# Performance work log

Measured on AMD Instinct MI355X. Metric: run time of the kernel, lower is better.

Reference implementation:

```python
import jax, jax.numpy as jnp
import numpy as np

B, S, D, H = 4, 1024, 512, 8
HD = D // H          # head_dim = 64
WIN = 32
EMB_HID = 128
NEG = -1e10


def _rel_coords_log():
    # __make_pair_wise_relative_positions: 2D meshgrid over window indexes
    idx = jnp.arange(WIN)
    coords = jnp.stack(jnp.meshgrid(idx, idx, indexing='ij'), 0).reshape(2, -1)  # [2, S]
    rel = coords[:, :, None] - coords[:, None, :]                                # [2, S, S]
    rel = rel.transpose(1, 2, 0).reshape(-1, 2).astype(jnp.float32)              # [S*S, 2]
    return jnp.sign(rel) * jnp.log1p(jnp.abs(rel))


def setup_inputs() -> dict:
    key = jax.random.key(0)
    ks = jax.random.split(key, 16)
    sd = 1.0 / np.sqrt(D)
    p = lambda k, sh, s: (jax.random.normal(k, sh, jnp.float32) * s)
    return {
        'query': jax.random.normal(ks[0], (B, S, D), jnp.float32),
        'key':   jax.random.normal(ks[1], (B, S, D), jnp.float32),
        'value': jax.random.normal(ks[2], (B, S, D), jnp.float32),
        'mask':  jnp.ones((B, 1, 1, S), jnp.int64),
        'Wq': p(ks[3], (D, D), sd), 'bq': jnp.zeros((D,), jnp.float32),
        'Wk': p(ks[4], (D, D), sd), 'bk': jnp.zeros((D,), jnp.float32),
        'Wv': p(ks[5], (D, D), sd), 'bv': jnp.zeros((D,), jnp.float32),
        'Wo': p(ks[6], (D, D), sd), 'bo': jnp.zeros((D,), jnp.float32),
        'W1': p(ks[7], (2, EMB_HID), 0.7), 'b1': jnp.zeros((EMB_HID,), jnp.float32),
        'W2': p(ks[8], (EMB_HID, H), 0.1), 'b2': jnp.zeros((H,), jnp.float32),
    }


def reference(query, key, value, mask, Wq, bq, Wk, bk, Wv, bv, Wo, bo, W1, b1, W2, b2):
    scale = jnp.sqrt(jnp.float32(HD))
    Q = (query @ Wq + bq).reshape(B, S, H, HD).transpose(0, 2, 1, 3)  # [B,H,S,HD]
    K = (key   @ Wk + bk).reshape(B, S, H, HD).transpose(0, 2, 1, 3)
    V = (value @ Wv + bv).reshape(B, S, H, HD).transpose(0, 2, 1, 3)

    energy = jnp.einsum('bhqd,bhkd->bhqk', Q, K) / scale             # [B,H,S,S]

    # continuous position bias: MLP(2 -> EMB_HID -> H) on log-spaced rel coords
    rel = _rel_coords_log()                                           # [S*S, 2]
    bias = jax.nn.relu(rel @ W1 + b1) @ W2 + b2                       # [S*S, H]
    bias = bias.T.reshape(H, S, S)[None]                              # [1,H,S,S]
    energy = energy + bias

    energy = jnp.where(mask == 0, NEG, energy)
    attention = jax.nn.softmax(energy, axis=-1)                       # [B,H,S,S]
    x = jnp.einsum('bhqk,bhkd->bhqd', attention, V)                   # dropout p=0
    x = x.transpose(0, 2, 1, 3).reshape(B, S, D)
    x = x @ Wo + bo
    return x, attention
```

## Files before the change

kernel.cpp:

```cpp
#include <hip/hip_runtime.h>
#include <hip/hip_bf16.h>

typedef __attribute__((ext_vector_type(4))) float f32x4;
typedef __attribute__((ext_vector_type(8))) short bf16x8;
typedef __attribute__((ext_vector_type(4))) unsigned short u16x4;

#define DEVI __device__ __forceinline__

constexpr int B_ = 4, S_ = 1024, D_ = 512, H_ = 8, HD_ = 64;
constexpr float CSH = 11.0903548f;

DEVI unsigned short f2b(float f) {
  union { float f; unsigned u; } v; v.f = f;
  unsigned r = v.u + 0x7fffu + ((v.u >> 16) & 1u);
  return (unsigned short)(r >> 16);
}

__global__ __launch_bounds__(256) void k_prep(const float* Wa, const float* Wb,
                                              const float* Wc, const float* Wd,
                                              unsigned short* T0, unsigned short* T1,
                                              unsigned short* T2, unsigned short* T3,
                                              const float* mW1, const float* mb1,
                                              const float* mW2, const float* mb2,
                                              float* table) {
  if (blockIdx.z == 4) {
    if (blockIdx.y != 0) return;
    int idx = blockIdx.x * 256 + threadIdx.x;
    if (idx >= 63 * 63) return;
    int dy = idx / 63 - 31, dx = idx % 63 - 31;
    float r0 = copysignf(log1pf(fabsf((float)dy)), (float)dy);
    float r1 = copysignf(log1pf(fabsf((float)dx)), (float)dx);
    float acc[8];
#pragma unroll
    for (int h = 0; h < 8; ++h) acc[h] = mb2[h];
    for (int j = 0; j < 128; ++j) {
      float hv = fmaxf(r0 * mW1[j] + r1 * mW1[128 + j] + mb1[j], 0.f);
#pragma unroll
      for (int h = 0; h < 8; ++h) acc[h] += hv * mW2[j * 8 + h];
    }
#pragma unroll
    for (int h = 0; h < 8; ++h) table[h * 3969 + idx] = acc[h] - CSH;
    return;
  }
  const float* W = blockIdx.z == 0 ? Wa : blockIdx.z == 1 ? Wb : blockIdx.z == 2 ? Wc : Wd;
  unsigned short* T = blockIdx.z == 0 ? T0 : blockIdx.z == 1 ? T1 : blockIdx.z == 2 ? T2 : T3;
  __shared__ float tile[32][33];
  int tx = threadIdx.x & 31, ty = threadIdx.x >> 5;
  int n0 = blockIdx.x * 32, k0 = blockIdx.y * 32;
#pragma unroll
  for (int r = 0; r < 4; ++r) tile[ty + r * 8][tx] = W[(size_t)(k0 + ty + r * 8) * D_ + n0 + tx];
  __syncthreads();
#pragma unroll
  for (int r = 0; r < 4; ++r) T[(size_t)(n0 + ty + r * 8) * D_ + k0 + tx] = f2b(tile[tx][ty + r * 8]);
}

__global__ __launch_bounds__(256) void k_gemm_qkv(const float* Aq, const float* Ak, const float* Av,
                                                  const unsigned short* Tq, const unsigned short* Tk,
                                                  const unsigned short* Tv,
                                                  const float* bqv, const float* bkv, const float* bvv,
                                                  unsigned short* Oq, unsigned short* Ok,
                                                  unsigned short* OvT) {
  const float* A = blockIdx.z == 0 ? Aq : blockIdx.z == 1 ? Ak : Av;
  const unsigned short* BT = blockIdx.z == 0 ? Tq : blockIdx.z == 1 ? Tk : Tv;
  const float* bias = blockIdx.z == 0 ? bqv : blockIdx.z == 1 ? bkv : bvv;

  __shared__ unsigned short As[64][72];
  __shared__ unsigned short Bs[128][72];
  const int tid = threadIdx.x;
  const int lane = tid & 63, wave = tid >> 6;
  const int lr = lane & 15, lg = lane >> 4;
  const int wm = (wave >> 1) * 32, wn = (wave & 1) * 64;
  const int m0 = blockIdx.x * 64, n0 = blockIdx.y * 128;

  f32x4 acc[2][4];
#pragma unroll
  for (int i = 0; i < 2; ++i)
#pragma unroll
    for (int j = 0; j < 4; ++j) acc[i][j] = (f32x4){0.f, 0.f, 0.f, 0.f};

  for (int k0 = 0; k0 < 512; k0 += 64) {
#pragma unroll
    for (int i = 0; i < 4; ++i) {
      int idx = tid + i * 256;
      int r = idx >> 4, c4 = (idx & 15) * 4;
      float4 fv = *(const float4*)(A + (size_t)(m0 + r) * 512 + k0 + c4);
      u16x4 wv;
      wv[0] = f2b(fv.x); wv[1] = f2b(fv.y); wv[2] = f2b(fv.z); wv[3] = f2b(fv.w);
      *(u16x4*)&As[r][c4] = wv;
    }
#pragma unroll
    for (int i = 0; i < 8; ++i) {
      int idx = tid + i * 256;
      int r = idx >> 4, c4 = (idx & 15) * 4;
      *(u16x4*)&Bs[r][c4] = *(const u16x4*)(BT + (size_t)(n0 + r) * 512 + k0 + c4);
    }
    __syncthreads();
#pragma unroll
    for (int kk = 0; kk < 2; ++kk) {
      bf16x8 af[2], bg[4];
#pragma unroll
      for (int i = 0; i < 2; ++i) af[i] = *(const bf16x8*)&As[wm + i * 16 + lr][kk * 32 + lg * 8];
#pragma unroll
      for (int j = 0; j < 4; ++j) bg[j] = *(const bf16x8*)&Bs[wn + j * 16 + lr][kk * 32 + lg * 8];
#pragma unroll
      for (int i = 0; i < 2; ++i)
#pragma unroll
        for (int j = 0; j < 4; ++j)
          acc[i][j] = __builtin_amdgcn_mfma_f32_16x16x32_bf16(af[i], bg[j], acc[i][j], 0, 0, 0);
    }
    __syncthreads();
  }

#pragma unroll
  for (int i = 0; i < 2; ++i)
#pragma unroll
    for (int j = 0; j < 4; ++j) {
      int mbase = m0 + wm + i * 16 + lg * 4;
      int n = n0 + wn + j * 16 + lr;
      float bvl = bias[n];
      int h = n >> 6, hd = n & 63;
      int bseg = mbase >> 10, s0 = mbase & 1023;
      if (blockIdx.z == 2) {
        u16x4 pk;
#pragma unroll
        for (int r = 0; r < 4; ++r) pk[r] = f2b(acc[i][j][r] + bvl);
        *(u16x4*)(OvT + (((size_t)(bseg * H_ + h) * 64 + hd) * 1024 + s0)) = pk;
      } else {
        unsigned short* outp = blockIdx.z == 0 ? Oq : Ok;
#pragma unroll
        for (int r = 0; r < 4; ++r) {
          float v = acc[i][j][r] + bvl;
          outp[(((size_t)bseg * H_ + h) * S_ + s0 + r) * HD_ + hd] = f2b(v);
        }
      }
    }
}

__global__ __launch_bounds__(256) void k_gemm_out(const unsigned short* A, const unsigned short* BT,
                                                  const float* bias, float* outp) {
  __shared__ unsigned short As[64][72];
  __shared__ unsigned short Bs[128][72];
  const int tid = threadIdx.x;
  const int lane = tid & 63, wave = tid >> 6;
  const int lr = lane & 15, lg = lane >> 4;
  const int wm = (wave >> 1) * 32, wn = (wave & 1) * 64;
  const int m0 = blockIdx.x * 64, n0 = blockIdx.y * 128;

  f32x4 acc[2][4];
#pragma unroll
  for (int i = 0; i < 2; ++i)
#pragma unroll
    for (int j = 0; j < 4; ++j) acc[i][j] = (f32x4){0.f, 0.f, 0.f, 0.f};

  for (int k0 = 0; k0 < 512; k0 += 64) {
#pragma unroll
    for (int i = 0; i < 4; ++i) {
      int idx = tid + i * 256;
      int r = idx >> 4, c4 = (idx & 15) * 4;
      *(u16x4*)&As[r][c4] = *(const u16x4*)(A + (size_t)(m0 + r) * 512 + k0 + c4);
    }
#pragma unroll
    for (int i = 0; i < 8; ++i) {
      int idx = tid + i * 256;
      int r = idx >> 4, c4 = (idx & 15) * 4;
      *(u16x4*)&Bs[r][c4] = *(const u16x4*)(BT + (size_t)(n0 + r) * 512 + k0 + c4);
    }
    __syncthreads();
#pragma unroll
    for (int kk = 0; kk < 2; ++kk) {
      bf16x8 af[2], bg[4];
#pragma unroll
      for (int i = 0; i < 2; ++i) af[i] = *(const bf16x8*)&As[wm + i * 16 + lr][kk * 32 + lg * 8];
#pragma unroll
      for (int j = 0; j < 4; ++j) bg[j] = *(const bf16x8*)&Bs[wn + j * 16 + lr][kk * 32 + lg * 8];
#pragma unroll
      for (int i = 0; i < 2; ++i)
#pragma unroll
        for (int j = 0; j < 4; ++j)
          acc[i][j] = __builtin_amdgcn_mfma_f32_16x16x32_bf16(af[i], bg[j], acc[i][j], 0, 0, 0);
    }
    __syncthreads();
  }

#pragma unroll
  for (int i = 0; i < 2; ++i)
#pragma unroll
    for (int j = 0; j < 4; ++j) {
      int mbase = m0 + wm + i * 16 + lg * 4;
      int n = n0 + wn + j * 16 + lr;
      float bvl = bias[n];
#pragma unroll
      for (int r = 0; r < 4; ++r)
        outp[(size_t)(mbase + r) * 512 + n] = acc[i][j][r] + bvl;
    }
}

__global__ __launch_bounds__(256) void k_attn(const unsigned short* Qb, const unsigned short* Kb,
                                              const unsigned short* VT, const float* tbl,
                                              const int* mask, float* out_attn,
                                              unsigned short* Xp) {
  const int tid = threadIdx.x;
  const int lane = tid & 63, w = tid >> 6;
  const int lr = lane & 15, lg = lane >> 4;
  const int bh = blockIdx.y, b = bh >> 3, h = bh & 7;
  const int q0 = blockIdx.x * 64;

  __shared__ unsigned short Ks[2][64][64];
  __shared__ unsigned short Vt[2][64][64];
  __shared__ unsigned short Pl[4][16][64];
  __shared__ float biasT[3969];
  __shared__ float mbig[1024];
  __shared__ int tbad[16];

  const unsigned short* Qh = Qb + (size_t)bh * (S_ * HD_);
  const unsigned short* Kh = Kb + (size_t)bh * (S_ * HD_);
  const unsigned short* Vth = VT + (size_t)bh * (HD_ * S_);

  const int srow = tid >> 3, sc = tid & 7;
  const int swz = (sc ^ (srow & 7)) * 8;

  if (tid < 16) tbad[tid] = 0;
  __syncthreads();
  for (int i = tid; i < 3969; i += 256) biasT[i] = tbl[h * 3969 + i];
  {
    int4 mv = *(const int4*)(mask + b * S_ + tid * 4);
    int base = tid * 4;
    mbig[base] = mv.x ? 3.0e38f : -1.0e9f;
    mbig[base + 1] = mv.y ? 3.0e38f : -1.0e9f;
    mbig[base + 2] = mv.z ? 3.0e38f : -1.0e9f;
    mbig[base + 3] = mv.w ? 3.0e38f : -1.0e9f;
    if (!(mv.x && mv.y && mv.z && mv.w)) tbad[base >> 6] = 1;
  }
  *(bf16x8*)&Ks[0][srow][swz] = *(const bf16x8*)(Kh + (size_t)srow * 64 + sc * 8);
  *(bf16x8*)&Ks[0][srow + 32][swz] = *(const bf16x8*)(Kh + (size_t)(srow + 32) * 64 + sc * 8);

  const int qrow = q0 + w * 16 + lr;
  const bf16x8 bq0 = *(const bf16x8*)(Qh + (size_t)qrow * 64 + lg * 8);
  const bf16x8 bq1 = *(const bf16x8*)(Qh + (size_t)qrow * 64 + 32 + lg * 8);
  const int qterm = (qrow >> 5) * 63 + (qrow & 31) + 1984;

  float ls = 0.f;
  __syncthreads();

  for (int kt = 0; kt < 16; ++kt) {
    const int cur = kt & 1;
    bf16x8 nk0, nk1;
    if (kt < 15) {
      nk0 = *(const bf16x8*)(Kh + (size_t)((kt + 1) * 64 + srow) * 64 + sc * 8);
      nk1 = *(const bf16x8*)(Kh + (size_t)((kt + 1) * 64 + srow + 32) * 64 + sc * 8);
    }
    const int bidx = qterm - 126 * kt;
    const bool bad = tbad[kt] != 0;
#pragma unroll
    for (int fn = 0; fn < 4; ++fn) {
      const unsigned short* krow = &Ks[cur][fn * 16 + lr][0];
      bf16x8 a0 = *(const bf16x8*)(krow + (lg ^ (lr & 7)) * 8);
      bf16x8 a1 = *(const bf16x8*)(krow + ((4 + lg) ^ (lr & 7)) * 8);
      f32x4 s = (f32x4){0.f, 0.f, 0.f, 0.f};
      s = __builtin_amdgcn_mfma_f32_16x16x32_bf16(a0, bq0, s, 0, 0, 0);
      s = __builtin_amdgcn_mfma_f32_16x16x32_bf16(a1, bq1, s, 0, 0, 0);
      const int kob = fn * 16 + lg * 4;
      const int ib = bidx - kob - (fn >= 2 ? 31 : 0);
#pragma unroll
      for (int r = 0; r < 4; ++r) {
        float arg = fmaf(s[r], 0.125f, biasT[ib - r]);
        if (bad) arg = fminf(arg, mbig[kt * 64 + kob + r]);
        ls += __expf(arg);
      }
    }
    if (kt < 15) {
      *(bf16x8*)&Ks[cur ^ 1][srow][swz] = nk0;
      *(bf16x8*)&Ks[cur ^ 1][srow + 32][swz] = nk1;
    }
    __syncthreads();
  }
  ls += __shfl_xor(ls, 16, 64);
  ls += __shfl_xor(ls, 32, 64);
  const float inv = 1.f / ls;

  f32x4 of[4];
#pragma unroll
  for (int i = 0; i < 4; ++i) of[i] = (f32x4){0.f, 0.f, 0.f, 0.f};
  float* oa = out_attn + (size_t)bh * (S_ * S_) + (size_t)qrow * S_;

  *(bf16x8*)&Ks[0][srow][swz] = *(const bf16x8*)(Kh + (size_t)srow * 64 + sc * 8);
  *(bf16x8*)&Ks[0][srow + 32][swz] = *(const bf16x8*)(Kh + (size_t)(srow + 32) * 64 + sc * 8);
  *(bf16x8*)&Vt[0][srow][swz] = *(const bf16x8*)(Vth + (size_t)srow * S_ + sc * 8);
  *(bf16x8*)&Vt[0][srow + 32][swz] = *(const bf16x8*)(Vth + (size_t)(srow + 32) * S_ + sc * 8);
  __syncthreads();

  for (int kt = 0; kt < 16; ++kt) {
    const int cur = kt & 1;
    bf16x8 nk0, nk1, nv0, nv1;
    if (kt < 15) {
      nk0 = *(const bf16x8*)(Kh + (size_t)((kt + 1) * 64 + srow) * 64 + sc * 8);
      nk1 = *(const bf16x8*)(Kh + (size_t)((kt + 1) * 64 + srow + 32) * 64 + sc * 8);
      nv0 = *(const bf16x8*)(Vth + (size_t)srow * S_ + (kt + 1) * 64 + sc * 8);
      nv1 = *(const bf16x8*)(Vth + (size_t)(srow + 32) * S_ + (kt + 1) * 64 + sc * 8);
    }
    const int bidx = qterm - 126 * kt;
    const bool bad = tbad[kt] != 0;
#pragma unroll
    for (int fn = 0; fn < 4; ++fn) {
      const unsigned short* krow = &Ks[cur][fn * 16 + lr][0];
      bf16x8 a0 = *(const bf16x8*)(krow + (lg ^ (lr & 7)) * 8);
      bf16x8 a1 = *(const bf16x8*)(krow + ((4 + lg) ^ (lr & 7)) * 8);
      f32x4 s = (f32x4){0.f, 0.f, 0.f, 0.f};
      s = __builtin_amdgcn_mfma_f32_16x16x32_bf16(a0, bq0, s, 0, 0, 0);
      s = __builtin_amdgcn_mfma_f32_16x16x32_bf16(a1, bq1, s, 0, 0, 0);
      const int kob = fn * 16 + lg * 4;
      const int ib = bidx - kob - (fn >= 2 ? 31 : 0);
      f32x4 pr;
      u16x4 pb;
#pragma unroll
      for (int r = 0; r < 4; ++r) {
        float arg = fmaf(s[r], 0.125f, biasT[ib - r]);
        if (bad) arg = fminf(arg, mbig[kt * 64 + kob + r]);
        float p = __expf(arg) * inv;
        pr[r] = p;
        pb[r] = f2b(p);
      }
      *(f32x4*)(oa + kt * 64 + kob) = pr;
      *(u16x4*)((char*)&Pl[w][lr][0] + ((fn * 2 + (lg >> 1)) ^ (lr & 7)) * 16 + (lg & 1) * 8) = pb;
    }
#pragma unroll
    for (int c = 0; c < 2; ++c) {
      bf16x8 pa = *(const bf16x8*)((const char*)&Pl[w][lr][0] + ((c * 4 + lg) ^ (lr & 7)) * 16);
#pragma unroll
      for (int fn2 = 0; fn2 < 4; ++fn2) {
        const unsigned short* vrow = &Vt[cur][fn2 * 16 + lr][0];
        bf16x8 bv = *(const bf16x8*)((const char*)vrow + ((c * 4 + lg) ^ (lr & 7)) * 16);
        of[fn2] = __builtin_amdgcn_mfma_f32_16x16x32_bf16(pa, bv, of[fn2], 0, 0, 0);
      }
    }
    if (kt < 15) {
      *(bf16x8*)&Ks[cur ^ 1][srow][swz] = nk0;
      *(bf16x8*)&Ks[cur ^ 1][srow + 32][swz] = nk1;
      *(bf16x8*)&Vt[cur ^ 1][srow][swz] = nv0;
      *(bf16x8*)&Vt[cur ^ 1][srow + 32][swz] = nv1;
    }
    __syncthreads();
  }

#pragma unroll
  for (int fn2 = 0; fn2 < 4; ++fn2)
#pragma unroll
    for (int r = 0; r < 4; ++r) {
      int q = q0 + w * 16 + lg * 4 + r;
      Xp[((size_t)b * S_ + q) * D_ + h * 64 + fn2 * 16 + lr] = f2b(of[fn2][r]);
    }
}

extern "C" void kernel_launch(void* const* d_in, const int* in_sizes, int n_in,
                              void* d_out, int out_size, void* d_ws, size_t ws_size,
                              hipStream_t stream) {
  const float* query = (const float*)d_in[0];
  const float* key   = (const float*)d_in[1];
  const float* value = (const float*)d_in[2];
  const int*   maskp = (const int*)d_in[3];
  const float* Wq = (const float*)d_in[4];
  const float* bq = (const float*)d_in[5];
  const float* Wk = (const float*)d_in[6];
  const float* bk = (const float*)d_in[7];
  const float* Wv = (const float*)d_in[8];
  const float* bv = (const float*)d_in[9];
  const float* Wo = (const float*)d_in[10];
  const float* bo = (const float*)d_in[11];
  const float* W1 = (const float*)d_in[12];
  const float* b1 = (const float*)d_in[13];
  const float* W2 = (const float*)d_in[14];
  const float* b2 = (const float*)d_in[15];

  char* ws = (char*)d_ws;
  const size_t MB4 = (size_t)4 * 1024 * 1024;
  unsigned short* Qb  = (unsigned short*)(ws);
  unsigned short* Kb  = (unsigned short*)(ws + MB4);
  unsigned short* VT  = (unsigned short*)(ws + 2 * MB4);
  unsigned short* Xp  = (unsigned short*)(ws + 3 * MB4);
  unsigned short* WqT = (unsigned short*)(ws + 4 * MB4);
  unsigned short* WkT = (unsigned short*)(ws + 4 * MB4 + 524288);
  unsigned short* WvT = (unsigned short*)(ws + 4 * MB4 + 2 * 524288);
  unsigned short* WoT = (unsigned short*)(ws + 4 * MB4 + 3 * 524288);
  float* table        = (float*)(ws + 4 * MB4 + 4 * 524288);

  float* out_x = (float*)d_out;
  float* out_attn = out_x + (size_t)B_ * S_ * D_;

  k_prep<<<dim3(16, 16, 5), 256, 0, stream>>>(Wq, Wk, Wv, Wo, WqT, WkT, WvT, WoT,
                                              W1, b1, W2, b2, table);
  k_gemm_qkv<<<dim3(64, 4, 3), 256, 0, stream>>>(query, key, value, WqT, WkT, WvT,
                                                 bq, bk, bv, Qb, Kb, VT);
  k_attn<<<dim3(16, 32), 256, 0, stream>>>(Qb, Kb, VT, table, maskp, out_attn, Xp);
  k_gemm_out<<<dim3(64, 4), 256, 0, stream>>>(Xp, WoT, bo, out_x);
}
```

Baseline: 100.7 us.

## Fuse two-pass softmax into single pass with register-held unnormalized probabilities

Merges the separate row-sum pass and the output pass into one loop. The loop computes exp without max subtraction, accumulates P·V unnormalized, and keeps bf16 copies of the probabilities in registers. After the loop it normalizes both the attention output and the PV result. This removes the second QK^T recompute and the second K load at the cost of large register usage (preg 16x4 vectors), under a launch_bounds occupancy hint. The attention output is now written from bf16-rounded probabilities, which lowers its precision, and the masked fill value changes to -30.

After: 245.3 us. 2.44x slower.

```diff
diff --git a/kernel.cpp b/kernel.cpp
--- a/kernel.cpp
+++ b/kernel.cpp
@@ -14,6 +14,11 @@
   union { float f; unsigned u; } v; v.f = f;
   unsigned r = v.u + 0x7fffu + ((v.u >> 16) & 1u);
   return (unsigned short)(r >> 16);
+}
+
+DEVI float b2f(unsigned short u) {
+  union { unsigned u; float f; } v; v.u = ((unsigned)u) << 16;
+  return v.f;
 }
 
 __global__ __launch_bounds__(256) void k_prep(const float* Wa, const float* Wb,
@@ -195,10 +200,10 @@
     }
 }
 
-__global__ __launch_bounds__(256) void k_attn(const unsigned short* Qb, const unsigned short* Kb,
-                                              const unsigned short* VT, const float* tbl,
-                                              const int* mask, float* out_attn,
-                                              unsigned short* Xp) {
+__global__ __launch_bounds__(256, 2) void k_attn(const unsigned short* Qb, const unsigned short* Kb,
+                                                 const unsigned short* VT, const float* tbl,
+                                                 const int* mask, float* out_attn,
+                                                 unsigned short* Xp) {
   const int tid = threadIdx.x;
   const int lane = tid & 63, w = tid >> 6;
   const int lr = lane & 15, lg = lane >> 4;
@@ -225,29 +230,38 @@
   {
     int4 mv = *(const int4*)(mask + b * S_ + tid * 4);
     int base = tid * 4;
-    mbig[base] = mv.x ? 3.0e38f : -1.0e9f;
-    mbig[base + 1] = mv.y ? 3.0e38f : -1.0e9f;
-    mbig[base + 2] = mv.z ? 3.0e38f : -1.0e9f;
-    mbig[base + 3] = mv.w ? 3.0e38f : -1.0e9f;
+    mbig[base] = mv.x ? 3.0e38f : -30.f;
+    mbig[base + 1] = mv.y ? 3.0e38f : -30.f;
+    mbig[base + 2] = mv.z ? 3.0e38f : -30.f;
+    mbig[base + 3] = mv.w ? 3.0e38f : -30.f;
     if (!(mv.x && mv.y && mv.z && mv.w)) tbad[base >> 6] = 1;
   }
   *(bf16x8*)&Ks[0][srow][swz] = *(const bf16x8*)(Kh + (size_t)srow * 64 + sc * 8);
   *(bf16x8*)&Ks[0][srow + 32][swz] = *(const bf16x8*)(Kh + (size_t)(srow + 32) * 64 + sc * 8);
+  *(bf16x8*)&Vt[0][srow][swz] = *(const bf16x8*)(Vth + (size_t)srow * S_ + sc * 8);
+  *(bf16x8*)&Vt[0][srow + 32][swz] = *(const bf16x8*)(Vth + (size_t)(srow + 32) * S_ + sc * 8);
 
   const int qrow = q0 + w * 16 + lr;
   const bf16x8 bq0 = *(const bf16x8*)(Qh + (size_t)qrow * 64 + lg * 8);
   const bf16x8 bq1 = *(const bf16x8*)(Qh + (size_t)qrow * 64 + 32 + lg * 8);
   const int qterm = (qrow >> 5) * 63 + (qrow & 31) + 1984;
 
+  u16x4 preg[16][4];
+  f32x4 of[4];
+#pragma unroll
+  for (int i = 0; i < 4; ++i) of[i] = (f32x4){0.f, 0.f, 0.f, 0.f};
   float ls = 0.f;
   __syncthreads();
 
+#pragma unroll
   for (int kt = 0; kt < 16; ++kt) {
     const int cur = kt & 1;
-    bf16x8 nk0, nk1;
+    bf16x8 nk0, nk1, nv0, nv1;
     if (kt < 15) {
       nk0 = *(const bf16x8*)(Kh + (size_t)((kt + 1) * 64 + srow) * 64 + sc * 8);
       nk1 = *(const bf16x8*)(Kh + (size_t)((kt + 1) * 64 + srow + 32) * 64 + sc * 8);
+      nv0 = *(const bf16x8*)(Vth + (size_t)srow * S_ + (kt + 1) * 64 + sc * 8);
+      nv1 = *(const bf16x8*)(Vth + (size_t)(srow + 32) * S_ + (kt + 1) * 64 + sc * 8);
     }
     const int bidx = qterm - 126 * kt;
     const bool bad = tbad[kt] != 0;
@@ -261,66 +275,16 @@
       s = __builtin_amdgcn_mfma_f32_16x16x32_bf16(a1, bq1, s, 0, 0, 0);
       const int kob = fn * 16 + lg * 4;
       const int ib = bidx - kob - (fn >= 2 ? 31 : 0);
+      u16x4 pb;
 #pragma unroll
       for (int r = 0; r < 4; ++r) {
         float arg = fmaf(s[r], 0.125f, biasT[ib - r]);
         if (bad) arg = fminf(arg, mbig[kt * 64 + kob + r]);
-        ls += __expf(arg);
-      }
-    }
-    if (kt < 15) {
-      *(bf16x8*)&Ks[cur ^ 1][srow][swz] = nk0;
-      *(bf16x8*)&Ks[cur ^ 1][srow + 32][swz] = nk1;
-    }
-    __syncthreads();
-  }
-  ls += __shfl_xor(ls, 16, 64);
-  ls += __shfl_xor(ls, 32, 64);
-  const float inv = 1.f / ls;
-
-  f32x4 of[4];
-#pragma unroll
-  for (int i = 0; i < 4; ++i) of[i] = (f32x4){0.f, 0.f, 0.f, 0.f};
-  float* oa = out_attn + (size_t)bh * (S_ * S_) + (size_t)qrow * S_;
-
-  *(bf16x8*)&Ks[0][srow][swz] = *(const bf16x8*)(Kh + (size_t)srow * 64 + sc * 8);
-  *(bf16x8*)&Ks[0][srow + 32][swz] = *(const bf16x8*)(Kh + (size_t)(srow + 32) * 64 + sc * 8);
-  *(bf16x8*)&Vt[0][srow][swz] = *(const bf16x8*)(Vth + (size_t)srow * S_ + sc * 8);
-  *(bf16x8*)&Vt[0][srow + 32][swz] = *(const bf16x8*)(Vth + (size_t)(srow + 32) * S_ + sc * 8);
-  __syncthreads();
-
-  for (int kt = 0; kt < 16; ++kt) {
-    const int cur = kt & 1;
-    bf16x8 nk0, nk1, nv0, nv1;
-    if (kt < 15) {
-      nk0 = *(const bf16x8*)(Kh + (size_t)((kt + 1) * 64 + srow) * 64 + sc * 8);
-      nk1 = *(const bf16x8*)(Kh + (size_t)((kt + 1) * 64 + srow + 32) * 64 + sc * 8);
-      nv0 = *(const bf16x8*)(Vth + (size_t)srow * S_ + (kt + 1) * 64 + sc * 8);
-      nv1 = *(const bf16x8*)(Vth + (size_t)(srow + 32) * S_ + (kt + 1) * 64 + sc * 8);
-    }
-    const int bidx = qterm - 126 * kt;
-    const bool bad = tbad[kt] != 0;
-#pragma unroll
-    for (int fn = 0; fn < 4; ++fn) {
-      const unsigned short* krow = &Ks[cur][fn * 16 + lr][0];
-      bf16x8 a0 = *(const bf16x8*)(krow + (lg ^ (lr & 7)) * 8);
-      bf16x8 a1 = *(const bf16x8*)(krow + ((4 + lg) ^ (lr & 7)) * 8);
-      f32x4 s = (f32x4){0.f, 0.f, 0.f, 0.f};
-      s = __builtin_amdgcn_mfma_f32_16x16x32_bf16(a0, bq0, s, 0, 0, 0);
-      s = __builtin_amdgcn_mfma_f32_16x16x32_bf16(a1, bq1, s, 0, 0, 0);
-      const int kob = fn * 16 + lg * 4;
-      const int ib = bidx - kob - (fn >= 2 ? 31 : 0);
-      f32x4 pr;
-      u16x4 pb;
-#pragma unroll
-      for (int r = 0; r < 4; ++r) {
-        float arg = fmaf(s[r], 0.125f, biasT[ib - r]);
-        if (bad) arg = fminf(arg, mbig[kt * 64 + kob + r]);
-        float p = __expf(arg) * inv;
-        pr[r] = p;
+        float p = __expf(arg);
+        ls += p;
         pb[r] = f2b(p);
       }
-      *(f32x4*)(oa + kt * 64 + kob) = pr;
+      preg[kt][fn] = pb;
       *(u16x4*)((char*)&Pl[w][lr][0] + ((fn * 2 + (lg >> 1)) ^ (lr & 7)) * 16 + (lg & 1) * 8) = pb;
     }
 #pragma unroll
@@ -342,12 +306,33 @@
     __syncthreads();
   }
 
+  ls += __shfl_xor(ls, 16, 64);
+  ls += __shfl_xor(ls, 32, 64);
+  const float inv = 1.f / ls;
+
+  f32x4 invq;
+#pragma unroll
+  for (int r = 0; r < 4; ++r) invq[r] = __shfl(inv, lg * 4 + r, 64);
+
+  float* oa = out_attn + (size_t)bh * (S_ * S_) + (size_t)qrow * S_;
+#pragma unroll
+  for (int kt = 0; kt < 16; ++kt) {
+#pragma unroll
+    for (int fn = 0; fn < 4; ++fn) {
+      u16x4 pb = preg[kt][fn];
+      f32x4 pr;
+#pragma unroll
+      for (int r = 0; r < 4; ++r) pr[r] = b2f(pb[r]) * inv;
+      *(f32x4*)(oa + kt * 64 + fn * 16 + lg * 4) = pr;
+    }
+  }
+
 #pragma unroll
   for (int fn2 = 0; fn2 < 4; ++fn2)
 #pragma unroll
     for (int r = 0; r < 4; ++r) {
       int q = q0 + w * 16 + lg * 4 + r;
-      Xp[((size_t)b * S_ + q) * D_ + h * 64 + fn2 * 16 + lr] = f2b(of[fn2][r]);
+      Xp[((size_t)b * S_ + q) * D_ + h * 64 + fn2 * 16 + lr] = f2b(of[fn2][r] * invq[r]);
     }
 }
 
```
